# Kernel optimization log

Measured on AMD Instinct MI355X. Metric: run time of the kernel, lower is better.

## Reference

```python
import jax, jax.numpy as jnp
import numpy as np

B, S, HID = 2, 8192, 1024
NH, DH, CL = 16, 64, 128
NB, NA = 1, 0  # num_chunks_before, num_chunks_after
NC = S // CL
MASK_VALUE = -1e9


def _look_adjacent(v):
    # v: [..., n_chunks, chunk_len(*d)] with chunk axis=2; torch's
    # cat([v[:,:,i:], v[:,:,:i]], dim=2) == jnp.roll(v, -i, axis=2)
    slices = [jnp.roll(v, -i, axis=2) for i in range(-NB, NA + 1)]
    return jnp.concatenate(slices, axis=3)


def setup_inputs() -> dict:
    key = jax.random.key(0)
    k1, k2, k3, k4 = jax.random.split(key, 4)
    scale = 1.0 / np.sqrt(HID).astype(np.float32)
    hidden_states = jax.random.normal(k1, (B, S, HID), jnp.float32)
    Wq = jax.random.normal(k2, (HID, NH * DH), jnp.float32) * scale
    Wk = jax.random.normal(k3, (HID, NH * DH), jnp.float32) * scale
    Wv = jax.random.normal(k4, (HID, NH * DH), jnp.float32) * scale
    return {"hidden_states": hidden_states, "Wq": Wq, "Wk": Wk, "Wv": Wv}


def _forward(hidden_states, Wq, Wk, Wv):
    # project and split heads -> [B, NH, NC, CL, DH]
    def proj(W):
        x = (hidden_states @ W).reshape(B, S, NH, DH)
        return x.transpose(0, 2, 1, 3).reshape(B, NH, NC, CL, DH)

    q = proj(Wq)
    k = proj(Wk) / jnp.sqrt(jnp.asarray(DH, hidden_states.dtype))
    v = proj(Wv)

    k_adj = _look_adjacent(k)  # [B, NH, NC, (NB+1+NA)*CL, DH]
    v_adj = _look_adjacent(v)

    # per-chunk scores: [B, NH, NC, CL, (NB+1+NA)*CL]
    dots = jnp.einsum("bhnqd,bhnkd->bhnqk", q, k_adj)

    # causal mask via position indices (decoder). Chunk 0's wrapped-around
    # keys carry large indices and are correctly masked out.
    idx = jnp.arange(S).reshape(1, 1, NC, CL)
    kv_idx = _look_adjacent(idx)  # [1, 1, NC, (NB+1+NA)*CL]
    causal = idx[..., :, None] >= kv_idx[..., None, :]
    dots = jnp.where(causal, dots, jnp.asarray(MASK_VALUE, dots.dtype))

    probs = jax.nn.softmax(dots, axis=-1)
    out = jnp.einsum("bhnqk,bhnkd->bhnqd", probs, v_adj)
    # merge chunks and heads -> [B, S, NH*DH]
    out = out.reshape(B, NH, S, DH).transpose(0, 2, 1, 3).reshape(B, S, NH * DH)
    return out


def reference(hidden_states, Wq, Wk, Wv):
    return _forward(hidden_states, Wq, Wk, Wv)
```

## Files before the change

kernel.cpp:

```cpp
#include <hip/hip_runtime.h>
#include <stdint.h>


typedef unsigned short u16;
typedef __bf16 bf16x8 __attribute__((ext_vector_type(8)));
typedef float f32x4 __attribute__((ext_vector_type(4)));

typedef __attribute__((address_space(1))) void* gas_ptr;
typedef __attribute__((address_space(3))) void* las_ptr;

__device__ __forceinline__ u16 f2bf(float f) {
  uint32_t u = __float_as_uint(f);
  u += 0x7fffu + ((u >> 16) & 1u);
  return (u16)(u >> 16);
}

__device__ __forceinline__ void gload16(const void* g, void* l) {
  __builtin_amdgcn_global_load_lds((gas_ptr)g, (las_ptr)l, 16, 0, 0);
}

__global__ void k_conv_x(const float* __restrict__ x, u16* __restrict__ o, int n4) {
  int i = blockIdx.x * blockDim.x + threadIdx.x;
  int stride = gridDim.x * blockDim.x;
  for (; i < n4; i += stride) {
    float4 v = reinterpret_cast<const float4*>(x)[i];
    unsigned long long pk = (unsigned long long)f2bf(v.x) |
                            ((unsigned long long)f2bf(v.y) << 16) |
                            ((unsigned long long)f2bf(v.z) << 32) |
                            ((unsigned long long)f2bf(v.w) << 48);
    reinterpret_cast<unsigned long long*>(o)[i] = pk;
  }
}

__global__ void k_conv_w(const float* __restrict__ wq, const float* __restrict__ wk,
                         const float* __restrict__ wv, u16* __restrict__ wt) {
  __shared__ float tile[32][33];
  int z = blockIdx.z;
  const float* src = (z == 0) ? wq : (z == 1) ? wk : wv;
  float scale = (z == 1) ? 0.125f : 1.0f;
  int n0 = blockIdx.x * 32, k0 = blockIdx.y * 32;
  int tx = threadIdx.x, ty = threadIdx.y;
  for (int i = ty; i < 32; i += 8)
    tile[i][tx] = src[(size_t)(k0 + i) * 1024 + n0 + tx];
  __syncthreads();
  u16* dst = wt + (size_t)z * 1024 * 1024;
  for (int i = ty; i < 32; i += 8)
    dst[(size_t)(n0 + i) * 1024 + k0 + tx] = f2bf(tile[tx][i] * scale);
}

template <int TR_OUT>
__global__ __launch_bounds__(512, 2) void k_gemm(const u16* __restrict__ xb,
                                                 const u16* __restrict__ wt,
                                                 u16* __restrict__ out) {
  __shared__ __align__(16) char lds[131072];
  char* As = lds;
  char* Bs = lds + 65536;
  const int tid = threadIdx.x;
  const int lane = tid & 63, l16 = lane & 15, lhi = lane >> 4;
  const int wave = tid >> 6;
  const int wm = (wave >> 2) * 128;
  const int wn = (wave & 3) * 64;
  const int bid = blockIdx.x;
  const int wg = (bid & 7) * 32 + (bid >> 3);
  const int m0 = (wg >> 2) * 256;
  const int n0 = (wg & 3) * 256;

  const int lrow8 = lane >> 3;
  const int scolx = ((lane & 7) * 16) ^ (lrow8 << 4);

  f32x4 acc[8][4] = {};

  auto stA = [&](int buf, int kt, int h) {
#pragma unroll
    for (int i = 0; i < 2; ++i) {
      int j = wave * 2 + i;
      int rb = 8 * j + 64 * (h + (j >> 3));
      int row = rb + lrow8;
      gload16((const char*)xb + ((size_t)(m0 + row) * 1024 + kt * 64) * 2 + scolx,
              As + buf * 32768 + rb * 128);
    }
  };
  auto stB = [&](int buf, int kt, int h) {
#pragma unroll
    for (int i = 0; i < 2; ++i) {
      int j = wave * 2 + i;
      int rb = 8 * (j & 3) + (j >> 2) * 64 + h * 32;
      int row = rb + lrow8;
      gload16((const char*)wt + ((size_t)(n0 + row) * 1024 + kt * 64) * 2 + scolx,
              Bs + buf * 32768 + rb * 128);
    }
  };

  stA(0, 0, 0); stB(0, 0, 0); stA(0, 0, 1); stB(0, 0, 1);

  for (int t = 0; t < 16; ++t) {
    const int cbuf = t & 1, nbuf = cbuf ^ 1;
    const int ktn = (t < 15) ? t + 1 : 15;
#pragma unroll
    for (int p = 0; p < 4; ++p) {
      __builtin_amdgcn_sched_barrier(0);
      if (p < 3) asm volatile("s_waitcnt vmcnt(4)" ::: "memory");
      __builtin_amdgcn_s_barrier();
      __builtin_amdgcn_sched_barrier(0);
      const int mh = p & 1, nh = p >> 1;
      bf16x8 af[4][2], bfr[2][2];
#pragma unroll
      for (int fi = 0; fi < 4; ++fi) {
        int row = wm + (mh * 4 + fi) * 16 + l16;
#pragma unroll
        for (int ks = 0; ks < 2; ++ks)
          af[fi][ks] = *(const bf16x8*)(As + cbuf * 32768 + row * 128 +
                                        ((ks * 64 + lhi * 16) ^ ((row & 7) << 4)));
      }
#pragma unroll
      for (int f2 = 0; f2 < 2; ++f2) {
        int rn = wn + nh * 32 + f2 * 16 + l16;
#pragma unroll
        for (int ks = 0; ks < 2; ++ks)
          bfr[f2][ks] = *(const bf16x8*)(Bs + cbuf * 32768 + rn * 128 +
                                         ((ks * 64 + lhi * 16) ^ ((rn & 7) << 4)));
      }
      if (p == 0) stA(nbuf, ktn, 0);
      else if (p == 1) stB(nbuf, ktn, 0);
      else if (p == 2) stA(nbuf, ktn, 1);
      else stB(nbuf, ktn, 1);
      asm volatile("s_waitcnt lgkmcnt(0)" ::: "memory");
      __builtin_amdgcn_sched_barrier(0);
      __builtin_amdgcn_s_setprio(1);
#pragma unroll
      for (int fi = 0; fi < 4; ++fi)
#pragma unroll
        for (int f2 = 0; f2 < 2; ++f2)
#pragma unroll
          for (int ks = 0; ks < 2; ++ks) {
            if constexpr (TR_OUT)
              acc[mh * 4 + fi][nh * 2 + f2] = __builtin_amdgcn_mfma_f32_16x16x32_bf16(
                  af[fi][ks], bfr[f2][ks], acc[mh * 4 + fi][nh * 2 + f2], 0, 0, 0);
            else
              acc[mh * 4 + fi][nh * 2 + f2] = __builtin_amdgcn_mfma_f32_16x16x32_bf16(
                  bfr[f2][ks], af[fi][ks], acc[mh * 4 + fi][nh * 2 + f2], 0, 0, 0);
          }
      __builtin_amdgcn_s_setprio(0);
    }
  }

  if constexpr (!TR_OUT) {
#pragma unroll
    for (int fr = 0; fr < 8; ++fr) {
#pragma unroll
      for (int fn = 0; fn < 4; ++fn) {
        int m = m0 + wm + fr * 16 + l16;
        int n = n0 + wn + fn * 16 + lhi * 4;
        unsigned long long pk = (unsigned long long)f2bf(acc[fr][fn][0]) |
                                ((unsigned long long)f2bf(acc[fr][fn][1]) << 16) |
                                ((unsigned long long)f2bf(acc[fr][fn][2]) << 32) |
                                ((unsigned long long)f2bf(acc[fr][fn][3]) << 48);
        *(unsigned long long*)((char*)out + ((size_t)m * 1024 + n) * 2) = pk;
      }
    }
  } else {
#pragma unroll
    for (int fr = 0; fr < 8; ++fr) {
#pragma unroll
      for (int fn = 0; fn < 4; ++fn) {
        int m = m0 + wm + fr * 16 + lhi * 4;
        int n = n0 + wn + fn * 16 + l16;
        int bb = m >> 13;
        int s = m & 8191;
        unsigned long long pk = (unsigned long long)f2bf(acc[fr][fn][0]) |
                                ((unsigned long long)f2bf(acc[fr][fn][1]) << 16) |
                                ((unsigned long long)f2bf(acc[fr][fn][2]) << 32) |
                                ((unsigned long long)f2bf(acc[fr][fn][3]) << 48);
        *(unsigned long long*)((char*)out + ((size_t)(bb * 1024 + n) * 8192 + s) * 2) = pk;
      }
    }
  }
}

__global__ __launch_bounds__(256, 2) void k_attn(const u16* __restrict__ qw,
                                                 const u16* __restrict__ kw,
                                                 const u16* __restrict__ vt,
                                                 float* __restrict__ out) {
  __shared__ __align__(16) char lds[81920];
  char* q_s = lds;
  char* k_s = lds + 16384;
  char* v_s = lds + 49152;
  const int tid = threadIdx.x;
  const int lane = tid & 63, l16 = lane & 15, lhi = lane >> 4;
  const int wave = tid >> 6;
  char* p_s = lds + wave * 8192;
  const int c = blockIdx.x & 63;
  const int h = (blockIdx.x >> 6) & 15;
  const int b = blockIdx.x >> 10;
  const int cprev = (c == 0) ? 0 : c - 1;
  const int dstb = (tid & 192) * 16;

#pragma unroll
  for (int it = 0; it < 4; ++it) {
    int idx = it * 256 + tid;
    int row = idx >> 3, colb = (idx & 7) * 16;
    gload16((const char*)qw + ((size_t)(b * 8192 + c * 128 + row) * 1024 + h * 64) * 2 +
                (colb ^ ((row & 7) << 4)),
            q_s + it * 4096 + dstb);
  }
#pragma unroll
  for (int it = 0; it < 8; ++it) {
    int idx = it * 256 + tid;
    int row = idx >> 3, colb = (idx & 7) * 16;
    int srow = (row < 128) ? (cprev * 128 + row) : (c * 128 + row - 128);
    gload16((const char*)kw + ((size_t)(b * 8192 + srow) * 1024 + h * 64) * 2 +
                (colb ^ ((row & 7) << 4)),
            k_s + it * 4096 + dstb);
  }
#pragma unroll
  for (int it = 0; it < 8; ++it) {
    int idx = it * 256 + tid;
    int row = idx >> 5;
    int colb = (idx & 31) * 16;
    int colbl = colb ^ ((row & 7) << 4);
    size_t roff = ((size_t)((b * 16 + h) * 64 + row)) * 8192 * 2;
    size_t soff = c ? ((size_t)(c * 128 - 128) * 2 + colbl) : (size_t)(colbl & 255);
    gload16((const char*)vt + roff + soff, v_s + it * 4096 + dstb);
  }
  __syncthreads();

  const int rbase = wave * 32;
  f32x4 accs[2][16];
#pragma unroll
  for (int rb = 0; rb < 2; ++rb)
#pragma unroll
    for (int nb = 0; nb < 16; ++nb) accs[rb][nb] = f32x4{0.f, 0.f, 0.f, 0.f};

#pragma unroll
  for (int ks = 0; ks < 2; ++ks) {
    bf16x8 af[2];
#pragma unroll
    for (int rb = 0; rb < 2; ++rb) {
      int row = rbase + rb * 16 + l16;
      af[rb] = *(const bf16x8*)(q_s + row * 128 + ((ks * 64 + lhi * 16) ^ ((row & 7) << 4)));
    }
#pragma unroll
    for (int nb = 0; nb < 16; ++nb) {
      int row = nb * 16 + l16;
      bf16x8 bfb = *(const bf16x8*)(k_s + row * 128 + ((ks * 64 + lhi * 16) ^ ((row & 7) << 4)));
#pragma unroll
      for (int rb = 0; rb < 2; ++rb)
        accs[rb][nb] = __builtin_amdgcn_mfma_f32_16x16x32_bf16(af[rb], bfb, accs[rb][nb], 0, 0, 0);
    }
  }

  float rinv[2][4];
#pragma unroll
  for (int rb = 0; rb < 2; ++rb) {
#pragma unroll
    for (int j = 0; j < 4; ++j) {
      int qi = rbase + rb * 16 + lhi * 4 + j;
      float m = -3.0e38f;
#pragma unroll
      for (int nb = 0; nb < 16; ++nb) {
        int kl = nb * 16 + l16;
        float v = accs[rb][nb][j];
        bool valid = (kl <= qi + 128) && ((c > 0) || (kl >= 128));
        v = valid ? v : -1.0e9f;
        accs[rb][nb][j] = v;
        m = fmaxf(m, v);
      }
#pragma unroll
      for (int d = 1; d < 16; d <<= 1) m = fmaxf(m, __shfl_xor(m, d));
      float s = 0.f;
#pragma unroll
      for (int nb = 0; nb < 16; ++nb) {
        float e = __expf(accs[rb][nb][j] - m);
        accs[rb][nb][j] = e;
        s += e;
      }
#pragma unroll
      for (int d = 1; d < 16; d <<= 1) s += __shfl_xor(s, d);
      rinv[rb][j] = 1.0f / s;
    }
  }

  __syncthreads();

  f32x4 acco[2][4] = {};
#pragma unroll
  for (int half = 0; half < 2; ++half) {
#pragma unroll
    for (int rb = 0; rb < 2; ++rb) {
#pragma unroll
      for (int nbh = 0; nbh < 8; ++nbh) {
#pragma unroll
        for (int j = 0; j < 4; ++j) {
          int r = rb * 16 + lhi * 4 + j;
          int cb = (nbh * 16 + l16) * 2;
          *(u16*)(p_s + r * 256 + (cb ^ ((r & 7) << 4))) = f2bf(accs[rb][half * 8 + nbh][j]);
        }
      }
    }
    __asm__ volatile("s_waitcnt lgkmcnt(0)" ::: "memory");
    __builtin_amdgcn_sched_barrier(0);
#pragma unroll
    for (int ks = 0; ks < 4; ++ks) {
      bf16x8 pf[2];
#pragma unroll
      for (int rb = 0; rb < 2; ++rb) {
        int r = rb * 16 + l16;
        pf[rb] = *(const bf16x8*)(p_s + r * 256 + ((ks * 64 + lhi * 16) ^ ((r & 7) << 4)));
      }
#pragma unroll
      for (int db = 0; db < 4; ++db) {
        int vr = db * 16 + l16;
        bf16x8 vf = *(const bf16x8*)(v_s + vr * 512 +
                                     ((half * 256 + ks * 64 + lhi * 16) ^ ((vr & 7) << 4)));
#pragma unroll
        for (int rb = 0; rb < 2; ++rb)
          acco[rb][db] = __builtin_amdgcn_mfma_f32_16x16x32_bf16(pf[rb], vf, acco[rb][db], 0, 0, 0);
      }
    }
    if (half == 0) {
      __asm__ volatile("s_waitcnt lgkmcnt(0)" ::: "memory");
      __builtin_amdgcn_sched_barrier(0);
    }
  }

#pragma unroll
  for (int rb = 0; rb < 2; ++rb) {
#pragma unroll
    for (int db = 0; db < 4; ++db) {
#pragma unroll
      for (int j = 0; j < 4; ++j) {
        int r = rbase + rb * 16 + lhi * 4 + j;
        out[(size_t)(b * 8192 + c * 128 + r) * 1024 + h * 64 + db * 16 + l16] =
            acco[rb][db][j] * rinv[rb][j];
      }
    }
  }
}

extern "C" void kernel_launch(void* const* d_in, const int* in_sizes, int n_in,
                              void* d_out, int out_size, void* d_ws, size_t ws_size,
                              hipStream_t stream) {
  const float* hs = (const float*)d_in[0];
  const float* wq = (const float*)d_in[1];
  const float* wk = (const float*)d_in[2];
  const float* wv = (const float*)d_in[3];
  float* out = (float*)d_out;
  char* ws = (char*)d_ws;

  u16* x_bf = (u16*)ws;
  u16* wt   = (u16*)(ws + 33554432);
  u16* q_ws = (u16*)(ws + 39845888);
  u16* k_ws = (u16*)(ws + 73400320);
  u16* v_t  = (u16*)(ws + 106954752);

  k_conv_x<<<dim3(2048), dim3(256), 0, stream>>>(hs, x_bf, 16384 * 1024 / 4);
  k_conv_w<<<dim3(32, 32, 3), dim3(32, 8), 0, stream>>>(wq, wk, wv, wt);
  k_gemm<0><<<dim3(256), dim3(512), 0, stream>>>(x_bf, wt, q_ws);
  k_gemm<0><<<dim3(256), dim3(512), 0, stream>>>(x_bf, wt + 1024 * 1024, k_ws);
  k_gemm<1><<<dim3(256), dim3(512), 0, stream>>>(x_bf, wt + 2 * 1024 * 1024, v_t);
  k_attn<<<dim3(2048), dim3(256), 0, stream>>>(q_ws, k_ws, v_t, out);
}
```

Baseline: 297.0 us.

## Fuse QKV projection GEMMs into one launch and stream Q/V from global in attention

The three separate Q, K and V projection GEMM launches become one 768-block kernel. Each block picks its weight matrix and output layout from the block index, and a runtime flag replaces the template parameter. The GEMM inner loop drops the per-phase vmcnt/lgkmcnt waits and barriers in favour of one __syncthreads per k-step. The attention kernel no longer stages Q and V in LDS: Q fragments are loaded into registers from global memory and V fragments are read from global inside the PV loop. This shrinks LDS to 32KB so launch bounds can allow 3 blocks per CU. The goals are less launch overhead and higher attention occupancy, at the risk of weaker GEMM pipelining and scattered global V reads.

```diff
diff --git a/kernel.cpp b/kernel.cpp
--- a/kernel.cpp
+++ b/kernel.cpp
@@ -48,10 +48,11 @@
     dst[(size_t)(n0 + i) * 1024 + k0 + tx] = f2bf(tile[tx][i] * scale);
 }
 
-template <int TR_OUT>
-__global__ __launch_bounds__(512, 2) void k_gemm(const u16* __restrict__ xb,
-                                                 const u16* __restrict__ wt,
-                                                 u16* __restrict__ out) {
+__global__ __launch_bounds__(512, 2) void k_gemmf(const u16* __restrict__ xb,
+                                                  const u16* __restrict__ wt,
+                                                  u16* __restrict__ q_ws,
+                                                  u16* __restrict__ k_ws,
+                                                  u16* __restrict__ v_t) {
   __shared__ __align__(16) char lds[131072];
   char* As = lds;
   char* Bs = lds + 65536;
@@ -60,10 +61,15 @@
   const int wave = tid >> 6;
   const int wm = (wave >> 2) * 128;
   const int wn = (wave & 3) * 64;
+
   const int bid = blockIdx.x;
-  const int wg = (bid & 7) * 32 + (bid >> 3);
-  const int m0 = (wg >> 2) * 256;
-  const int n0 = (wg & 3) * 256;
+  const int wg = (bid & 7) * 96 + (bid >> 3);
+  const int mp = wg / 12;
+  const int np = wg % 12;
+  const int z = np >> 2;
+  const int m0 = mp * 256;
+  const int n0 = (np & 3) * 256;
+  const u16* wz = wt + (size_t)z * 1024 * 1024;
 
   const int lrow8 = lane >> 3;
   const int scolx = ((lane & 7) * 16) ^ (lrow8 << 4);
@@ -86,24 +92,22 @@
       int j = wave * 2 + i;
       int rb = 8 * (j & 3) + (j >> 2) * 64 + h * 32;
       int row = rb + lrow8;
-      gload16((const char*)wt + ((size_t)(n0 + row) * 1024 + kt * 64) * 2 + scolx,
+      gload16((const char*)wz + ((size_t)(n0 + row) * 1024 + kt * 64) * 2 + scolx,
               Bs + buf * 32768 + rb * 128);
     }
   };
 
   stA(0, 0, 0); stB(0, 0, 0); stA(0, 0, 1); stB(0, 0, 1);
+
+  const bool swapped = (z < 2);
 
   for (int t = 0; t < 16; ++t) {
     const int cbuf = t & 1, nbuf = cbuf ^ 1;
     const int ktn = (t < 15) ? t + 1 : 15;
-#pragma unroll
-    for (int p = 0; p < 4; ++p) {
-      __builtin_amdgcn_sched_barrier(0);
-      if (p < 3) asm volatile("s_waitcnt vmcnt(4)" ::: "memory");
-      __builtin_amdgcn_s_barrier();
-      __builtin_amdgcn_sched_barrier(0);
-      const int mh = p & 1, nh = p >> 1;
-      bf16x8 af[4][2], bfr[2][2];
+    __syncthreads();
+#pragma unroll
+    for (int mh = 0; mh < 2; ++mh) {
+      bf16x8 af[4][2];
 #pragma unroll
       for (int fi = 0; fi < 4; ++fi) {
         int row = wm + (mh * 4 + fi) * 16 + l16;
@@ -113,38 +117,48 @@
                                         ((ks * 64 + lhi * 16) ^ ((row & 7) << 4)));
       }
 #pragma unroll
-      for (int f2 = 0; f2 < 2; ++f2) {
-        int rn = wn + nh * 32 + f2 * 16 + l16;
-#pragma unroll
-        for (int ks = 0; ks < 2; ++ks)
-          bfr[f2][ks] = *(const bf16x8*)(Bs + cbuf * 32768 + rn * 128 +
-                                         ((ks * 64 + lhi * 16) ^ ((rn & 7) << 4)));
-      }
-      if (p == 0) stA(nbuf, ktn, 0);
-      else if (p == 1) stB(nbuf, ktn, 0);
-      else if (p == 2) stA(nbuf, ktn, 1);
-      else stB(nbuf, ktn, 1);
-      asm volatile("s_waitcnt lgkmcnt(0)" ::: "memory");
-      __builtin_amdgcn_sched_barrier(0);
-      __builtin_amdgcn_s_setprio(1);
-#pragma unroll
-      for (int fi = 0; fi < 4; ++fi)
-#pragma unroll
-        for (int f2 = 0; f2 < 2; ++f2)
-#pragma unroll
-          for (int ks = 0; ks < 2; ++ks) {
-            if constexpr (TR_OUT)
-              acc[mh * 4 + fi][nh * 2 + f2] = __builtin_amdgcn_mfma_f32_16x16x32_bf16(
-                  af[fi][ks], bfr[f2][ks], acc[mh * 4 + fi][nh * 2 + f2], 0, 0, 0);
-            else
-              acc[mh * 4 + fi][nh * 2 + f2] = __builtin_amdgcn_mfma_f32_16x16x32_bf16(
-                  bfr[f2][ks], af[fi][ks], acc[mh * 4 + fi][nh * 2 + f2], 0, 0, 0);
-          }
-      __builtin_amdgcn_s_setprio(0);
-    }
-  }
-
-  if constexpr (!TR_OUT) {
+      for (int nh = 0; nh < 2; ++nh) {
+        bf16x8 bfr[2][2];
+#pragma unroll
+        for (int f2 = 0; f2 < 2; ++f2) {
+          int rn = wn + nh * 32 + f2 * 16 + l16;
+#pragma unroll
+          for (int ks = 0; ks < 2; ++ks)
+            bfr[f2][ks] = *(const bf16x8*)(Bs + cbuf * 32768 + rn * 128 +
+                                           ((ks * 64 + lhi * 16) ^ ((rn & 7) << 4)));
+        }
+        int p = mh * 2 + nh;
+        if (p == 0) stA(nbuf, ktn, 0);
+        else if (p == 1) stB(nbuf, ktn, 0);
+        else if (p == 2) stA(nbuf, ktn, 1);
+        else stB(nbuf, ktn, 1);
+        __builtin_amdgcn_s_setprio(1);
+        if (swapped) {
+#pragma unroll
+          for (int fi = 0; fi < 4; ++fi)
+#pragma unroll
+            for (int f2 = 0; f2 < 2; ++f2)
+#pragma unroll
+              for (int ks = 0; ks < 2; ++ks)
+                acc[mh * 4 + fi][nh * 2 + f2] = __builtin_amdgcn_mfma_f32_16x16x32_bf16(
+                    bfr[f2][ks], af[fi][ks], acc[mh * 4 + fi][nh * 2 + f2], 0, 0, 0);
+        } else {
+#pragma unroll
+          for (int fi = 0; fi < 4; ++fi)
+#pragma unroll
+            for (int f2 = 0; f2 < 2; ++f2)
+#pragma unroll
+              for (int ks = 0; ks < 2; ++ks)
+                acc[mh * 4 + fi][nh * 2 + f2] = __builtin_amdgcn_mfma_f32_16x16x32_bf16(
+                    af[fi][ks], bfr[f2][ks], acc[mh * 4 + fi][nh * 2 + f2], 0, 0, 0);
+        }
+        __builtin_amdgcn_s_setprio(0);
+      }
+    }
+  }
+
+  if (swapped) {
+    u16* o = (z == 0) ? q_ws : k_ws;
 #pragma unroll
     for (int fr = 0; fr < 8; ++fr) {
 #pragma unroll
@@ -155,7 +169,7 @@
                                 ((unsigned long long)f2bf(acc[fr][fn][1]) << 16) |
                                 ((unsigned long long)f2bf(acc[fr][fn][2]) << 32) |
                                 ((unsigned long long)f2bf(acc[fr][fn][3]) << 48);
-        *(unsigned long long*)((char*)out + ((size_t)m * 1024 + n) * 2) = pk;
+        *(unsigned long long*)((char*)o + ((size_t)m * 1024 + n) * 2) = pk;
       }
     }
   } else {
@@ -171,20 +185,18 @@
                                 ((unsigned long long)f2bf(acc[fr][fn][1]) << 16) |
                                 ((unsigned long long)f2bf(acc[fr][fn][2]) << 32) |
                                 ((unsigned long long)f2bf(acc[fr][fn][3]) << 48);
-        *(unsigned long long*)((char*)out + ((size_t)(bb * 1024 + n) * 8192 + s) * 2) = pk;
-      }
-    }
-  }
-}
-
-__global__ __launch_bounds__(256, 2) void k_attn(const u16* __restrict__ qw,
+        *(unsigned long long*)((char*)v_t + ((size_t)(bb * 1024 + n) * 8192 + s) * 2) = pk;
+      }
+    }
+  }
+}
+
+__global__ __launch_bounds__(256, 3) void k_attn(const u16* __restrict__ qw,
                                                  const u16* __restrict__ kw,
                                                  const u16* __restrict__ vt,
                                                  float* __restrict__ out) {
-  __shared__ __align__(16) char lds[81920];
-  char* q_s = lds;
-  char* k_s = lds + 16384;
-  char* v_s = lds + 49152;
+  __shared__ __align__(16) char lds[32768];
+  char* k_s = lds;
   const int tid = threadIdx.x;
   const int lane = tid & 63, l16 = lane & 15, lhi = lane >> 4;
   const int wave = tid >> 6;
@@ -196,14 +208,6 @@
   const int dstb = (tid & 192) * 16;
 
 #pragma unroll
-  for (int it = 0; it < 4; ++it) {
-    int idx = it * 256 + tid;
-    int row = idx >> 3, colb = (idx & 7) * 16;
-    gload16((const char*)qw + ((size_t)(b * 8192 + c * 128 + row) * 1024 + h * 64) * 2 +
-                (colb ^ ((row & 7) << 4)),
-            q_s + it * 4096 + dstb);
-  }
-#pragma unroll
   for (int it = 0; it < 8; ++it) {
     int idx = it * 256 + tid;
     int row = idx >> 3, colb = (idx & 7) * 16;
@@ -212,19 +216,19 @@
                 (colb ^ ((row & 7) << 4)),
             k_s + it * 4096 + dstb);
   }
-#pragma unroll
-  for (int it = 0; it < 8; ++it) {
-    int idx = it * 256 + tid;
-    int row = idx >> 5;
-    int colb = (idx & 31) * 16;
-    int colbl = colb ^ ((row & 7) << 4);
-    size_t roff = ((size_t)((b * 16 + h) * 64 + row)) * 8192 * 2;
-    size_t soff = c ? ((size_t)(c * 128 - 128) * 2 + colbl) : (size_t)(colbl & 255);
-    gload16((const char*)vt + roff + soff, v_s + it * 4096 + dstb);
-  }
+
+  const int rbase = wave * 32;
+  bf16x8 qf[2][2];
+#pragma unroll
+  for (int rb = 0; rb < 2; ++rb)
+#pragma unroll
+    for (int ks = 0; ks < 2; ++ks)
+      qf[rb][ks] = *(const bf16x8*)((const char*)qw +
+                                    ((size_t)(b * 8192 + c * 128 + rbase + rb * 16 + l16)) * 2048 +
+                                    h * 128 + ks * 64 + lhi * 16);
+
   __syncthreads();
 
-  const int rbase = wave * 32;
   f32x4 accs[2][16];
 #pragma unroll
   for (int rb = 0; rb < 2; ++rb)
@@ -233,19 +237,13 @@
 
 #pragma unroll
   for (int ks = 0; ks < 2; ++ks) {
-    bf16x8 af[2];
-#pragma unroll
-    for (int rb = 0; rb < 2; ++rb) {
-      int row = rbase + rb * 16 + l16;
-      af[rb] = *(const bf16x8*)(q_s + row * 128 + ((ks * 64 + lhi * 16) ^ ((row & 7) << 4)));
-    }
 #pragma unroll
     for (int nb = 0; nb < 16; ++nb) {
       int row = nb * 16 + l16;
       bf16x8 bfb = *(const bf16x8*)(k_s + row * 128 + ((ks * 64 + lhi * 16) ^ ((row & 7) << 4)));
 #pragma unroll
       for (int rb = 0; rb < 2; ++rb)
-        accs[rb][nb] = __builtin_amdgcn_mfma_f32_16x16x32_bf16(af[rb], bfb, accs[rb][nb], 0, 0, 0);
+        accs[rb][nb] = __builtin_amdgcn_mfma_f32_16x16x32_bf16(qf[rb][ks], bfb, accs[rb][nb], 0, 0, 0);
     }
   }
 
@@ -310,8 +308,10 @@
 #pragma unroll
       for (int db = 0; db < 4; ++db) {
         int vr = db * 16 + l16;
-        bf16x8 vf = *(const bf16x8*)(v_s + vr * 512 +
-                                     ((half * 256 + ks * 64 + lhi * 16) ^ ((vr & 7) << 4)));
+        size_t koffb = c ? ((size_t)(c - 1) * 256 + half * 256 + ks * 64 + lhi * 16)
+                         : (size_t)((half * 256 + ks * 64 + lhi * 16) & 255);
+        bf16x8 vf = *(const bf16x8*)((const char*)vt +
+                                     ((size_t)((b * 16 + h) * 64 + vr)) * 16384 + koffb);
 #pragma unroll
         for (int rb = 0; rb < 2; ++rb)
           acco[rb][db] = __builtin_amdgcn_mfma_f32_16x16x32_bf16(pf[rb], vf, acco[rb][db], 0, 0, 0);
@@ -355,8 +355,6 @@
 
   k_conv_x<<<dim3(2048), dim3(256), 0, stream>>>(hs, x_bf, 16384 * 1024 / 4);
   k_conv_w<<<dim3(32, 32, 3), dim3(32, 8), 0, stream>>>(wq, wk, wv, wt);
-  k_gemm<0><<<dim3(256), dim3(512), 0, stream>>>(x_bf, wt, q_ws);
-  k_gemm<0><<<dim3(256), dim3(512), 0, stream>>>(x_bf, wt + 1024 * 1024, k_ws);
-  k_gemm<1><<<dim3(256), dim3(512), 0, stream>>>(x_bf, wt + 2 * 1024 * 1024, v_t);
+  k_gemmf<<<dim3(768), dim3(512), 0, stream>>>(x_bf, wt, q_ws, k_ws, v_t);
   k_attn<<<dim3(2048), dim3(256), 0, stream>>>(q_ws, k_ws, v_t, out);
 }
```

Result: slower. 344.6 us (+16.0%).
